# Optimization experiments

Hardware: AMD Instinct MI355X
Metric: run time of the kernel (lower is better)

The kernel has to match this reference:

```python
import jax, jax.numpy as jnp
import numpy as np

NUM_HEAD = 8

def conv1x1(x, W, b):
    # x: (n, c, h, w); W: (o, c); b: (o,)
    return jnp.einsum('nchw,oc->nohw', x, W) + b[None, :, None, None]

def setup_inputs() -> dict:
    key = jax.random.key(0)
    ks = jax.random.split(key, 9)
    n, C, H, Wd = 16, 512, 64, 64
    KC, VC = 256, 512
    s = lambda fan_in: 1.0 / np.sqrt(fan_in)
    return {
        'x':  jax.random.normal(ks[0], (n, C, H, Wd), dtype=jnp.float32),
        'Wk': jax.random.normal(ks[1], (KC, C), dtype=jnp.float32) * s(C),
        'bk': jnp.zeros((KC,), dtype=jnp.float32),
        'Wq': jax.random.normal(ks[2], (KC, C), dtype=jnp.float32) * s(C),
        'bq': jnp.zeros((KC,), dtype=jnp.float32),
        'Wv': jax.random.normal(ks[3], (VC, C), dtype=jnp.float32) * s(C),
        'bv': jnp.zeros((VC,), dtype=jnp.float32),
        'We': jax.random.normal(ks[4], (C, VC), dtype=jnp.float32) * s(VC),
        'be': jnp.zeros((C,), dtype=jnp.float32),
    }

def reference(x, Wk, bk, Wq, bq, Wv, bv, We, be):
    n, c, h, w = x.shape
    L = h * w
    Hn = NUM_HEAD
    key   = conv1x1(x, Wk, bk).reshape(n, Hn, -1, L)   # (n, H, hk, L)
    query = conv1x1(x, Wq, bq).reshape(n, Hn, -1, L)   # (n, H, hk, L)
    value = conv1x1(x, Wv, bv).reshape(n, Hn, -1, L)   # (n, H, hv, L)
    key_sm   = jax.nn.softmax(key, axis=3)              # softmax over spatial
    query_sm = jax.nn.softmax(query, axis=2)            # softmax over head channels
    # linear attention: (value @ key^T) @ query, no LxL matrix
    context = jnp.einsum('nhvl,nhkl->nhvk', value, key_sm)     # (n, H, hv, hk)
    att = jnp.einsum('nhvk,nhkl->nhvl', context, query_sm)     # (n, H, hv, L)
    att = att.reshape(n, -1, h, w)                              # (n, VC, h, w)
    return x + conv1x1(att, We, be)
```

## Files before the change

kernel.cpp:

```cpp
#include <hip/hip_runtime.h>
#include <cstddef>
#include <cstdint>

#define N_BATCH 16
#define C_IN    512
#define L       4096
#define KC      256
#define VC      512
#define NH      8
#define HK      32
#define HV      64

using f32x4 = __attribute__((ext_vector_type(4))) float;
using s16x8 = __attribute__((ext_vector_type(8))) short;

static __device__ inline ushort f2bf(float f) {
  uint32_t u = __float_as_uint(f);
  uint32_t r = (u + 0x7FFFu + ((u >> 16) & 1u)) >> 16;
  return (ushort)r;
}
static __device__ inline float bf2f(ushort u) {
  return __uint_as_float((uint32_t)u << 16);
}

__global__ __launch_bounds__(256) void k_prep_w(
    const float* __restrict__ Wk, const float* __restrict__ bk,
    const float* __restrict__ Wq, const float* __restrict__ bq,
    ushort* __restrict__ Wb, float* __restrict__ bb)
{
  const int o = blockIdx.x;
  const float* src; const float* bsrc; int oo;
  if (o < 256) { src = Wk + (size_t)o * C_IN;         bsrc = bk; oo = o; }
  else         { src = Wq + (size_t)(o - 256) * C_IN; bsrc = bq; oo = o - 256; }
  const int t = threadIdx.x;
  Wb[(size_t)o * C_IN + t * 2]     = f2bf(src[t * 2]);
  Wb[(size_t)o * C_IN + t * 2 + 1] = f2bf(src[t * 2 + 1]);
  if (t == 0) bb[o] = bsrc[oo];
}

__global__ __launch_bounds__(256) void k_prep_x(const float* __restrict__ x,
                                                ushort* __restrict__ xT,
                                                ushort* __restrict__ xb)
{
  __shared__ float t[64][65];
  const int n = blockIdx.z, cy = blockIdx.y, lx = blockIdx.x;
  const float* xp = x + ((size_t)n * C_IN + cy * 64) * L + (size_t)lx * 64;
  ushort* xbp = xb + ((size_t)n * C_IN + cy * 64) * L + (size_t)lx * 64;
  const int l4 = (threadIdx.x & 15) * 4;
  const int c0 = threadIdx.x >> 4;
  #pragma unroll
  for (int i = 0; i < 4; ++i) {
    int cc = c0 + i * 16;
    f32x4 v = *(const f32x4*)&xp[(size_t)cc * L + l4];
    t[cc][l4]     = v[0];
    t[cc][l4 + 1] = v[1];
    t[cc][l4 + 2] = v[2];
    t[cc][l4 + 3] = v[3];
    uint2 pk;
    pk.x = (uint32_t)f2bf(v[0]) | ((uint32_t)f2bf(v[1]) << 16);
    pk.y = (uint32_t)f2bf(v[2]) | ((uint32_t)f2bf(v[3]) << 16);
    *(uint2*)(xbp + (size_t)cc * L + l4) = pk;
  }
  __syncthreads();
  ushort* op = xT + ((size_t)n * L + lx * 64) * C_IN + cy * 64;
  const int cp = (threadIdx.x & 15) * 4;
  const int l0 = threadIdx.x >> 4;
  #pragma unroll
  for (int i = 0; i < 4; ++i) {
    int lr = l0 + i * 16;
    uint2 pk;
    pk.x = (uint32_t)f2bf(t[cp][lr])     | ((uint32_t)f2bf(t[cp + 1][lr]) << 16);
    pk.y = (uint32_t)f2bf(t[cp + 2][lr]) | ((uint32_t)f2bf(t[cp + 3][lr]) << 16);
    *(uint2*)(op + (size_t)lr * C_IN + cp) = pk;
  }
}

#define QBM 256
#define QBN 256
#define QBK 64

__global__ __launch_bounds__(512) void k_kq_mfma(
    const ushort* __restrict__ Wb,
    const ushort* __restrict__ xT,
    const float* __restrict__ bb,
    ushort* __restrict__ Kbuf,
    ushort* __restrict__ qT)
{
  extern __shared__ __align__(16) char smem[];
  const int n  = blockIdx.z;
  const int oy = blockIdx.y;
  const int lx = blockIdx.x;
  const int tid  = threadIdx.x;
  const int wave = tid >> 6, lane = tid & 63;
  const int wr = wave >> 2, wc = wave & 3;

  f32x4 acc[8][4] = {};

  const ushort* gA = Wb + (size_t)(oy * QBM) * C_IN;
  const ushort* gB = xT + ((size_t)n * L + lx * QBN) * C_IN;

  const int srow = lane >> 3;
  const int sslotbase = lane & 7;

  #define QSTAGE(buf, k0)                                                        \
    {                                                                            \
      ushort* As_ = (ushort*)(smem + (buf) * 65536);                             \
      ushort* Bs_ = (ushort*)(smem + (buf) * 65536 + 32768);                     \
      _Pragma("unroll")                                                          \
      for (int i_ = 0; i_ < 4; ++i_) {                                           \
        int rbase_ = wave * 32 + i_ * 8;                                         \
        int row_ = rbase_ + srow;                                                \
        int ss_ = sslotbase ^ (row_ & 7);                                        \
        __builtin_amdgcn_global_load_lds(                                        \
            (const __attribute__((address_space(1))) uint32_t*)(gA + (size_t)row_ * C_IN + (k0) + ss_ * 8), \
            (__attribute__((address_space(3))) uint32_t*)(As_ + rbase_ * QBK),   \
            16, 0, 0);                                                           \
        __builtin_amdgcn_global_load_lds(                                        \
            (const __attribute__((address_space(1))) uint32_t*)(gB + (size_t)row_ * C_IN + (k0) + ss_ * 8), \
            (__attribute__((address_space(3))) uint32_t*)(Bs_ + rbase_ * QBK),   \
            16, 0, 0);                                                           \
      }                                                                          \
    }

  QSTAGE(0, 0)
  __syncthreads();

  const int nt = C_IN / QBK;
  for (int t = 0; t < nt; ++t) {
    if (t < nt - 1) QSTAGE((t + 1) & 1, (t + 1) * QBK)
    ushort* As = (ushort*)(smem + (t & 1) * 65536);
    ushort* Bs = (ushort*)(smem + (t & 1) * 65536 + 32768);
    __builtin_amdgcn_s_setprio(1);
    #pragma unroll
    for (int ks = 0; ks < 2; ++ks) {
      s16x8 af[8], bfr[4];
      #pragma unroll
      for (int m = 0; m < 8; ++m) {
        int row = wr * 128 + m * 16 + (lane & 15);
        int slot = (ks * 4 + (lane >> 4)) ^ (row & 7);
        af[m] = *(const s16x8*)&As[row * QBK + slot * 8];
      }
      #pragma unroll
      for (int nn = 0; nn < 4; ++nn) {
        int row = wc * 64 + nn * 16 + (lane & 15);
        int slot = (ks * 4 + (lane >> 4)) ^ (row & 7);
        bfr[nn] = *(const s16x8*)&Bs[row * QBK + slot * 8];
      }
      #pragma unroll
      for (int m = 0; m < 8; ++m)
        #pragma unroll
        for (int nn = 0; nn < 4; ++nn)
          acc[m][nn] = __builtin_amdgcn_mfma_f32_16x16x32_bf16(af[m], bfr[nn], acc[m][nn], 0, 0, 0);
    }
    __builtin_amdgcn_s_setprio(0);
    __syncthreads();
  }
  #undef QSTAGE

  if (oy == 0) {
    float* ep = (float*)smem + wave * (16 * 68);
    const int erow = lane >> 4;
    const int ecol = lane & 15;
    const float* bias = bb + wr * 128;
    ushort* outp = Kbuf + ((size_t)n * 256 + wr * 128) * L
                 + (size_t)lx * QBN + wc * 64;
    #pragma unroll
    for (int m = 0; m < 8; ++m) {
      #pragma unroll
      for (int nn = 0; nn < 4; ++nn)
        #pragma unroll
        for (int r = 0; r < 4; ++r)
          ep[(erow * 4 + r) * 68 + nn * 16 + ecol] = acc[m][nn][r];
      #pragma unroll
      for (int p = 0; p < 4; ++p) {
        int row = p * 4 + erow;
        f32x4 v = *(const f32x4*)&ep[row * 68 + ecol * 4];
        float bo = bias[m * 16 + row];
        uint2 pk;
        pk.x = (uint32_t)f2bf(v[0] + bo) | ((uint32_t)f2bf(v[1] + bo) << 16);
        pk.y = (uint32_t)f2bf(v[2] + bo) | ((uint32_t)f2bf(v[3] + bo) << 16);
        *(uint2*)&outp[(size_t)(m * 16 + row) * L + ecol * 4] = pk;
      }
    }
  } else {
    const float* bias = bb + 256 + wr * 128;
    ushort* qbase = qT + (size_t)n * L * KC;
    const int g4 = (lane >> 4) * 4;
    #pragma unroll
    for (int hp = 0; hp < 4; ++hp) {
      const int m0 = 2 * hp, m1 = 2 * hp + 1;
      const float b0_0 = bias[m0 * 16 + g4 + 0], b0_1 = bias[m0 * 16 + g4 + 1];
      const float b0_2 = bias[m0 * 16 + g4 + 2], b0_3 = bias[m0 * 16 + g4 + 3];
      const float b1_0 = bias[m1 * 16 + g4 + 0], b1_1 = bias[m1 * 16 + g4 + 1];
      const float b1_2 = bias[m1 * 16 + g4 + 2], b1_3 = bias[m1 * 16 + g4 + 3];
      #pragma unroll
      for (int nn = 0; nn < 4; ++nn) {
        float v0[4], v1[4];
        v0[0] = acc[m0][nn][0] + b0_0; v0[1] = acc[m0][nn][1] + b0_1;
        v0[2] = acc[m0][nn][2] + b0_2; v0[3] = acc[m0][nn][3] + b0_3;
        v1[0] = acc[m1][nn][0] + b1_0; v1[1] = acc[m1][nn][1] + b1_1;
        v1[2] = acc[m1][nn][2] + b1_2; v1[3] = acc[m1][nn][3] + b1_3;
        float mx = fmaxf(fmaxf(fmaxf(v0[0], v0[1]), fmaxf(v0[2], v0[3])),
                         fmaxf(fmaxf(v1[0], v1[1]), fmaxf(v1[2], v1[3])));
        mx = fmaxf(mx, __shfl_xor(mx, 16));
        mx = fmaxf(mx, __shfl_xor(mx, 32));
        float e0[4], e1[4];
        float s = 0.f;
        #pragma unroll
        for (int r = 0; r < 4; ++r) { e0[r] = __expf(v0[r] - mx); s += e0[r]; }
        #pragma unroll
        for (int r = 0; r < 4; ++r) { e1[r] = __expf(v1[r] - mx); s += e1[r]; }
        s += __shfl_xor(s, 16);
        s += __shfl_xor(s, 32);
        float inv = 1.0f / s;
        int l = lx * QBN + wc * 64 + nn * 16 + (lane & 15);
        ushort* dst = qbase + (size_t)l * KC + wr * 128;
        uint2 p0, p1;
        p0.x = (uint32_t)f2bf(e0[0] * inv) | ((uint32_t)f2bf(e0[1] * inv) << 16);
        p0.y = (uint32_t)f2bf(e0[2] * inv) | ((uint32_t)f2bf(e0[3] * inv) << 16);
        p1.x = (uint32_t)f2bf(e1[0] * inv) | ((uint32_t)f2bf(e1[1] * inv) << 16);
        p1.y = (uint32_t)f2bf(e1[2] * inv) | ((uint32_t)f2bf(e1[3] * inv) << 16);
        *(uint2*)&dst[m0 * 16 + g4] = p0;
        *(uint2*)&dst[m1 * 16 + g4] = p1;
      }
    }
  }
}

__device__ inline float blockReduceMax(float v, float* red) {
  #pragma unroll
  for (int off = 32; off > 0; off >>= 1)
    v = fmaxf(v, __shfl_down(v, off, 64));
  int tid = threadIdx.x;
  if ((tid & 63) == 0) red[tid >> 6] = v;
  __syncthreads();
  return fmaxf(fmaxf(red[0], red[1]), fmaxf(red[2], red[3]));
}
__device__ inline float blockReduceSum(float v, float* red) {
  #pragma unroll
  for (int off = 32; off > 0; off >>= 1)
    v += __shfl_down(v, off, 64);
  int tid = threadIdx.x;
  if ((tid & 63) == 0) red[tid >> 6] = v;
  __syncthreads();
  return red[0] + red[1] + red[2] + red[3];
}

__global__ __launch_bounds__(256) void k_kstats3(const ushort* __restrict__ Kbuf,
                                                 float* __restrict__ kmax,
                                                 float* __restrict__ kinv)
{
  const int r = blockIdx.x;
  const int n = blockIdx.y;
  const ushort* row = Kbuf + ((size_t)n * 256 + r) * L;
  __shared__ float red1[4];
  __shared__ float red2[4];
  const int tid = threadIdx.x;
  s16x8 a = *(const s16x8*)(row + tid * 16);
  s16x8 b = *(const s16x8*)(row + tid * 16 + 8);
  float v[16];
  #pragma unroll
  for (int j = 0; j < 8; ++j) { v[j] = bf2f((ushort)a[j]); v[8 + j] = bf2f((ushort)b[j]); }
  float m = -3.0e38f;
  #pragma unroll
  for (int j = 0; j < 16; ++j) m = fmaxf(m, v[j]);
  m = blockReduceMax(m, red1);
  float s = 0.f;
  #pragma unroll
  for (int j = 0; j < 16; ++j) s += __expf(v[j] - m);
  s = blockReduceSum(s, red2);
  if (tid == 0) { kmax[n * KC + r] = m; kinv[n * KC + r] = 1.0f / s; }
}

#define GBK 64

__global__ __launch_bounds__(512) void k_G(
    const ushort* __restrict__ xb,
    const ushort* __restrict__ Kbuf,
    const float* __restrict__ kmax,
    const float* __restrict__ kinv,
    float* __restrict__ Gp)
{
  extern __shared__ __align__(16) char smem[];
  const int cm = blockIdx.x;
  const int lc = blockIdx.y;
  const int n  = blockIdx.z;
  const int tid  = threadIdx.x;
  const int wave = tid >> 6, lane = tid & 63;
  const int wr = wave >> 2, wc = wave & 3;

  f32x4 acc[4][4] = {};

  const ushort* gxb = xb   + ((size_t)n * C_IN + cm * 128) * L + lc * 1024;
  const ushort* gK  = Kbuf + (size_t)n * 256 * L + lc * 1024;

  const int brow = tid >> 1;
  const int bseg0 = (tid & 1) * 4;
  const float mk = kmax[n * KC + brow];
  const float ik = kinv[n * KC + brow];

  #define ASTAGE(buf, k0)                                                        \
    {                                                                            \
      ushort* As_ = (ushort*)(smem + (buf) * 49152);                             \
      _Pragma("unroll")                                                          \
      for (int i_ = 0; i_ < 2; ++i_) {                                           \
        int rbase_ = wave * 16 + i_ * 8;                                         \
        int row_ = rbase_ + (lane >> 3);                                         \
        int ss_ = (lane & 7) ^ (row_ & 7);                                       \
        __builtin_amdgcn_global_load_lds(                                        \
            (const __attribute__((address_space(1))) uint32_t*)(gxb + (size_t)row_ * L + (k0) + ss_ * 8), \
            (__attribute__((address_space(3))) uint32_t*)(As_ + rbase_ * GBK),   \
            16, 0, 0);                                                           \
      }                                                                          \
    }

  #define BLOAD(k0)                                                              \
    _Pragma("unroll")                                                            \
    for (int i_ = 0; i_ < 4; ++i_)                                               \
      bk[i_] = *(const s16x8*)(gK + (size_t)brow * L + (k0) + (bseg0 + i_) * 8);

  #define BWRITE(buf)                                                            \
    {                                                                            \
      ushort* Bs_ = (ushort*)(smem + (buf) * 49152 + 16384);                     \
      _Pragma("unroll")                                                          \
      for (int i_ = 0; i_ < 4; ++i_) {                                           \
        s16x8 w_;                                                                \
        _Pragma("unroll")                                                        \
        for (int j_ = 0; j_ < 8; ++j_)                                           \
          w_[j_] = (short)f2bf(__expf(bf2f((ushort)bk[i_][j_]) - mk) * ik);      \
        *(s16x8*)&Bs_[brow * GBK + ((bseg0 + i_) ^ (brow & 7)) * 8] = w_;        \
      }                                                                          \
    }

  s16x8 bk[4];

  BLOAD(0)
  ASTAGE(0, 0)
  BWRITE(0)
  __syncthreads();

  const int nt = 1024 / GBK;
  for (int t = 0; t < nt; ++t) {
    const int cb = t & 1, nb = cb ^ 1;
    if (t < nt - 1) {
      BLOAD((t + 1) * GBK)
      ASTAGE(nb, (t + 1) * GBK)
    }
    ushort* As = (ushort*)(smem + cb * 49152);
    ushort* Bs = (ushort*)(smem + cb * 49152 + 16384);
    __builtin_amdgcn_s_setprio(1);
    #pragma unroll
    for (int ks = 0; ks < 2; ++ks) {
      s16x8 af[4], bfr[4];
      #pragma unroll
      for (int m = 0; m < 4; ++m) {
        int row = wr * 64 + m * 16 + (lane & 15);
        int slot = (ks * 4 + (lane >> 4)) ^ (row & 7);
        af[m] = *(const s16x8*)&As[row * GBK + slot * 8];
      }
      #pragma unroll
      for (int nn = 0; nn < 4; ++nn) {
        int row = wc * 64 + nn * 16 + (lane & 15);
        int slot = (ks * 4 + (lane >> 4)) ^ (row & 7);
        bfr[nn] = *(const s16x8*)&Bs[row * GBK + slot * 8];
      }
      #pragma unroll
      for (int m = 0; m < 4; ++m)
        #pragma unroll
        for (int nn = 0; nn < 4; ++nn)
          acc[m][nn] = __builtin_amdgcn_mfma_f32_16x16x32_bf16(af[m], bfr[nn], acc[m][nn], 0, 0, 0);
    }
    __builtin_amdgcn_s_setprio(0);
    if (t < nt - 1) BWRITE(nb)
    __syncthreads();
  }
  #undef ASTAGE
  #undef BLOAD
  #undef BWRITE

  float* ep = (float*)smem + wave * (16 * 68);
  const int erow = lane >> 4;
  const int ecol = lane & 15;
  float* op = Gp + (((size_t)n * 4 + lc) * 512 + cm * 128 + wr * 64) * 256 + wc * 64;
  #pragma unroll
  for (int m = 0; m < 4; ++m) {
    #pragma unroll
    for (int nn = 0; nn < 4; ++nn)
      #pragma unroll
      for (int r = 0; r < 4; ++r)
        ep[(erow * 4 + r) * 68 + nn * 16 + ecol] = acc[m][nn][r];
    #pragma unroll
    for (int p = 0; p < 4; ++p) {
      int row16 = p * 4 + erow;
      f32x4 v = *(const f32x4*)&ep[row16 * 68 + ecol * 4];
      *(f32x4*)&op[(size_t)(m * 16 + row16) * 256 + ecol * 4] = v;
    }
  }
}

__global__ __launch_bounds__(256) void k_F(
    const float* __restrict__ Wv, const float* __restrict__ bv,
    const float* __restrict__ We,
    ushort* __restrict__ F, float* __restrict__ Fb)
{
  const int h  = blockIdx.x;
  const int og = blockIdx.y;
  const int tid = threadIdx.x;
  __shared__ float Ws[16][64];
  #pragma unroll
  for (int i = 0; i < 4; ++i) {
    int e = tid + i * 256;
    int o = e >> 6, v = e & 63;
    Ws[o][v] = We[(size_t)(og * 16 + o) * VC + h * 64 + v];
  }
  __syncthreads();
  const int c2 = tid * 2;
  float acc[16][2] = {};
  for (int v = 0; v < 64; ++v) {
    float2 w = *(const float2*)&Wv[(size_t)(h * 64 + v) * C_IN + c2];
    #pragma unroll
    for (int o = 0; o < 16; ++o) {
      acc[o][0] += Ws[o][v] * w.x;
      acc[o][1] += Ws[o][v] * w.y;
    }
  }
  ushort* Fh = F + ((size_t)h * 512 + og * 16) * C_IN;
  #pragma unroll
  for (int o = 0; o < 16; ++o) {
    uint32_t pk = (uint32_t)f2bf(acc[o][0]) | ((uint32_t)f2bf(acc[o][1]) << 16);
    *(uint32_t*)&Fh[(size_t)o * C_IN + c2] = pk;
  }
  if (tid < 16) {
    float s = 0.f;
    for (int v = 0; v < 64; ++v) s += Ws[tid][v] * bv[h * 64 + v];
    Fb[h * 512 + og * 16 + tid] = s;
  }
}

__global__ __launch_bounds__(256) void k_M(
    const float* __restrict__ Gp,
    const ushort* __restrict__ F,
    const float* __restrict__ Fb,
    ushort* __restrict__ Mbuf)
{
  const int oy = blockIdx.x;
  const int h  = blockIdx.y;
  const int n  = blockIdx.z;
  const int tid = threadIdx.x, wave = tid >> 6, lane = tid & 63;

  __shared__ __align__(16) char smem[32768 + 32768 + 9216];
  ushort* GTs = (ushort*)smem;

  #pragma unroll
  for (int i = 0; i < 16; ++i) {
    int e = tid + i * 256;
    int c = e >> 3, kq = e & 7;
    int k = kq * 4;
    const float* gp = Gp + ((size_t)n * 4 * 512 + c) * 256 + h * HK + k;
    f32x4 s = *(const f32x4*)gp;
    s += *(const f32x4*)(gp + (size_t)512 * 256);
    s += *(const f32x4*)(gp + (size_t)2 * 512 * 256);
    s += *(const f32x4*)(gp + (size_t)3 * 512 * 256);
    #pragma unroll
    for (int j = 0; j < 4; ++j) {
      int kk = k + j;
      GTs[kk * 512 + (((c >> 3) ^ (kk & 7)) * 8) + (c & 7)] = f2bf(s[j]);
    }
  }

  const ushort* gA = F + ((size_t)h * 512 + oy * 128) * C_IN;

  #define MSTAGE(buf, k0)                                                        \
    {                                                                            \
      ushort* As_ = (ushort*)(smem + 32768 + (buf) * 16384);                     \
      _Pragma("unroll")                                                          \
      for (int i_ = 0; i_ < 4; ++i_) {                                           \
        int rbase_ = wave * 32 + i_ * 8;                                         \
        int row_ = rbase_ + (lane >> 3);                                         \
        int ss_ = (lane & 7) ^ (row_ & 7);                                       \
        __builtin_amdgcn_global_load_lds(                                        \
            (const __attribute__((address_space(1))) uint32_t*)(gA + (size_t)row_ * C_IN + (k0) + ss_ * 8), \
            (__attribute__((address_space(3))) uint32_t*)(As_ + rbase_ * 64),    \
            16, 0, 0);                                                           \
      }                                                                          \
    }

  f32x4 acc[2][2] = {};

  MSTAGE(0, 0)
  __syncthreads();

  const int nt = C_IN / 64;
  for (int t = 0; t < nt; ++t) {
    if (t < nt - 1) MSTAGE((t + 1) & 1, (t + 1) * 64)
    ushort* As = (ushort*)(smem + 32768 + (t & 1) * 16384);
    __builtin_amdgcn_s_setprio(1);
    #pragma unroll
    for (int ks = 0; ks < 2; ++ks) {
      s16x8 af[2], bfr[2];
      #pragma unroll
      for (int m = 0; m < 2; ++m) {
        int row = wave * 32 + m * 16 + (lane & 15);
        int slot = (ks * 4 + (lane >> 4)) ^ (row & 7);
        af[m] = *(const s16x8*)&As[row * 64 + slot * 8];
      }
      #pragma unroll
      for (int nf = 0; nf < 2; ++nf) {
        int kr = nf * 16 + (lane & 15);
        int slot = (t * 8 + ks * 4 + (lane >> 4)) ^ (kr & 7);
        bfr[nf] = *(const s16x8*)&GTs[kr * 512 + slot * 8];
      }
      #pragma unroll
      for (int m = 0; m < 2; ++m)
        #pragma unroll
        for (int nf = 0; nf < 2; ++nf)
          acc[m][nf] = __builtin_amdgcn_mfma_f32_16x16x32_bf16(af[m], bfr[nf], acc[m][nf], 0, 0, 0);
    }
    __builtin_amdgcn_s_setprio(0);
    __syncthreads();
  }
  #undef MSTAGE

  float* ep = (float*)(smem + 65536) + wave * (16 * 36);
  const int erow = lane >> 4;
  const int ecol = lane & 15;
  #pragma unroll
  for (int m = 0; m < 2; ++m) {
    #pragma unroll
    for (int nf = 0; nf < 2; ++nf)
      #pragma unroll
      for (int r = 0; r < 4; ++r)
        ep[(erow * 4 + r) * 36 + nf * 16 + ecol] = acc[m][nf][r];
    #pragma unroll
    for (int p = 0; p < 2; ++p) {
      int row16 = p * 8 + (lane >> 3);
      int c4 = (lane & 7) * 4;
      f32x4 v = *(const f32x4*)&ep[row16 * 36 + c4];
      int o = oy * 128 + wave * 32 + m * 16 + row16;
      float fb = Fb[h * 512 + o];
      uint2 pk;
      pk.x = (uint32_t)f2bf(v[0] + fb) | ((uint32_t)f2bf(v[1] + fb) << 16);
      pk.y = (uint32_t)f2bf(v[2] + fb) | ((uint32_t)f2bf(v[3] + fb) << 16);
      *(uint2*)&Mbuf[((size_t)n * 512 + o) * KC + h * HK + c4] = pk;
    }
  }
}

#define BM 128
#define BN 128
#define BK 32

__global__ __launch_bounds__(256) void k_final_mfma(
    const ushort* __restrict__ Mb,
    const ushort* __restrict__ qT,
    const float* __restrict__ x,
    const float* __restrict__ be,
    float* __restrict__ out)
{
  const int n  = blockIdx.z;
  const int oy = blockIdx.y;
  const int lx = blockIdx.x;
  const int tid  = threadIdx.x;
  const int wave = tid >> 6, lane = tid & 63;
  const int wr = wave >> 1, wc = wave & 1;

  __shared__ __align__(16) char smem[32768 + 17408];

  f32x4 acc[4][4] = {};

  const ushort* gA = Mb + ((size_t)n * 512 + oy * BM) * KC;
  const ushort* gB = qT + ((size_t)n * L + lx * BN) * KC;

  const int r0 = wave * 32;
  const int lrow = lane >> 2;

  #define FSTAGE(buf, k0)                                                        \
    {                                                                            \
      ushort* As_ = (ushort*)(smem + (buf) * 16384);                             \
      ushort* Bs_ = (ushort*)(smem + (buf) * 16384 + 8192);                      \
      _Pragma("unroll")                                                          \
      for (int i_ = 0; i_ < 2; ++i_) {                                           \
        int row_ = r0 + i_ * 16 + lrow;                                          \
        int ss_ = (lane & 3) ^ ((row_ >> 1) & 3);                                \
        __builtin_amdgcn_global_load_lds(                                        \
            (const __attribute__((address_space(1))) uint32_t*)(gA + (size_t)row_ * KC + (k0) + ss_ * 8), \
            (__attribute__((address_space(3))) uint32_t*)(As_ + (r0 + i_ * 16) * BK), \
            16, 0, 0);                                                           \
        __builtin_amdgcn_global_load_lds(                                        \
            (const __attribute__((address_space(1))) uint32_t*)(gB + (size_t)row_ * KC + (k0) + ss_ * 8), \
            (__attribute__((address_space(3))) uint32_t*)(Bs_ + (r0 + i_ * 16) * BK), \
            16, 0, 0);                                                           \
      }                                                                          \
    }

  FSTAGE(0, 0)
  __syncthreads();

  const int nt = KC / BK;
  for (int t = 0; t < nt; ++t) {
    if (t < nt - 1) FSTAGE((t + 1) & 1, (t + 1) * BK)
    ushort* As = (ushort*)(smem + (t & 1) * 16384);
    ushort* Bs = (ushort*)(smem + (t & 1) * 16384 + 8192);
    s16x8 af[4], bfr[4];
    #pragma unroll
    for (int m = 0; m < 4; ++m) {
      int row = wr * 64 + m * 16 + (lane & 15);
      int slot = (lane >> 4) ^ ((row >> 1) & 3);
      af[m] = *(const s16x8*)&As[row * BK + slot * 8];
    }
    #pragma unroll
    for (int nn = 0; nn < 4; ++nn) {
      int row = wc * 64 + nn * 16 + (lane & 15);
      int slot = (lane >> 4) ^ ((row >> 1) & 3);
      bfr[nn] = *(const s16x8*)&Bs[row * BK + slot * 8];
    }
    __builtin_amdgcn_s_setprio(1);
    #pragma unroll
    for (int m = 0; m < 4; ++m)
      #pragma unroll
      for (int nn = 0; nn < 4; ++nn)
        acc[m][nn] = __builtin_amdgcn_mfma_f32_16x16x32_bf16(af[m], bfr[nn], acc[m][nn], 0, 0, 0);
    __builtin_amdgcn_s_setprio(0);
    __syncthreads();
  }
  #undef FSTAGE

  float* ep = (float*)(smem + 32768) + wave * (16 * 68);
  const int erow = lane >> 4;
  const int ecol = lane & 15;
  const float* bias = be + oy * BM + wr * 64;
  const float* xp = x + ((size_t)n * 512 + oy * BM + wr * 64) * L
                  + (size_t)lx * BN + wc * 64;
  float* op = out + ((size_t)n * 512 + oy * BM + wr * 64) * L
            + (size_t)lx * BN + wc * 64;
  #pragma unroll
  for (int m = 0; m < 4; ++m) {
    #pragma unroll
    for (int nn = 0; nn < 4; ++nn)
      #pragma unroll
      for (int r = 0; r < 4; ++r)
        ep[(erow * 4 + r) * 68 + nn * 16 + ecol] = acc[m][nn][r];
    #pragma unroll
    for (int p = 0; p < 4; ++p) {
      int row = p * 4 + erow;
      f32x4 v = *(const f32x4*)&ep[row * 68 + ecol * 4];
      float bo = bias[m * 16 + row];
      f32x4 xv = *(const f32x4*)&xp[(size_t)(m * 16 + row) * L + ecol * 4];
      v = v + xv + bo;
      *(f32x4*)&op[(size_t)(m * 16 + row) * L + ecol * 4] = v;
    }
  }
}

extern "C" void kernel_launch(void* const* d_in, const int* in_sizes, int n_in,
                              void* d_out, int out_size, void* d_ws, size_t ws_size,
                              hipStream_t stream)
{
  const float* x  = (const float*)d_in[0];
  const float* Wk = (const float*)d_in[1];
  const float* bk = (const float*)d_in[2];
  const float* Wq = (const float*)d_in[3];
  const float* bq = (const float*)d_in[4];
  const float* Wv = (const float*)d_in[5];
  const float* bv = (const float*)d_in[6];
  const float* We = (const float*)d_in[7];
  const float* be = (const float*)d_in[8];
  float* out = (float*)d_out;

  char* ws = (char*)d_ws;
  size_t off = 0;
  ushort* Kbuf = (ushort*)(ws + off); off += (size_t)N_BATCH * 256 * L * 2;
  ushort* xT   = (ushort*)(ws + off); off += (size_t)N_BATCH * L * C_IN * 2;
  ushort* xb   = (ushort*)(ws + off); off += (size_t)N_BATCH * C_IN * L * 2;
  ushort* Wb   = (ushort*)(ws + off); off += (size_t)512 * C_IN * 2;
  float*  bb   = (float*)(ws + off);  off += (size_t)512 * 4;
  float*  kmax = (float*)(ws + off);  off += (size_t)N_BATCH * KC * 4;
  float*  kinv = (float*)(ws + off);  off += (size_t)N_BATCH * KC * 4;
  ushort* qT   = (ushort*)(ws + off); off += (size_t)N_BATCH * L * KC * 2;
  float*  Gp   = (float*)(ws + off);  off += (size_t)N_BATCH * 4 * 512 * 256 * 4;
  ushort* Fbuf = (ushort*)(ws + off); off += (size_t)NH * 512 * C_IN * 2;
  float*  Fb   = (float*)(ws + off);  off += (size_t)NH * 512 * 4;
  ushort* Mbuf = (ushort*)(ws + off); off += (size_t)N_BATCH * 512 * KC * 2;

  (void)hipFuncSetAttribute((const void*)k_kq_mfma,
                            hipFuncAttributeMaxDynamicSharedMemorySize, 131072);
  (void)hipFuncSetAttribute((const void*)k_G,
                            hipFuncAttributeMaxDynamicSharedMemorySize, 98304);

  k_prep_w<<<dim3(512), 256, 0, stream>>>(Wk, bk, Wq, bq, Wb, bb);
  k_F<<<dim3(NH, 32), 256, 0, stream>>>(Wv, bv, We, Fbuf, Fb);
  k_prep_x<<<dim3(64, 8, N_BATCH), 256, 0, stream>>>(x, xT, xb);
  k_kq_mfma<<<dim3(16, 2, N_BATCH), 512, 131072, stream>>>(Wb, xT, bb, Kbuf, qT);
  k_kstats3<<<dim3(KC, N_BATCH), 256, 0, stream>>>(Kbuf, kmax, kinv);
  k_G<<<dim3(4, 4, N_BATCH), 512, 98304, stream>>>(xb, Kbuf, kmax, kinv, Gp);
  k_M<<<dim3(4, NH, N_BATCH), 256, 0, stream>>>(Gp, Fbuf, Fb, Mbuf);
  k_final_mfma<<<dim3(32, 4, N_BATCH), 256, 0, stream>>>(Mbuf, qT, x, be, out);
}
```

Before: 268.0 us.

## Drop transposed x copy; use LDS transpose reads in K/Q GEMM

Removes the transposed bf16 copy xT and makes the x preparation kernel a plain elementwise fp32-to-bf16 conversion. The K/Q GEMM now stages B tiles directly from the channel-major xb layout and builds MFMA operands with ds_read_b64_tr_b16 transpose reads from LDS. This removes one full write of the activation tensor and the shared-memory transpose pass. In exchange it adds an explicit lgkmcnt wait and a scheduling barrier inside the inner loop, and the new LDS layout could cause bank conflicts.

```diff
diff --git a/kernel.cpp b/kernel.cpp
--- a/kernel.cpp
+++ b/kernel.cpp
@@ -13,6 +13,8 @@
 
 using f32x4 = __attribute__((ext_vector_type(4))) float;
 using s16x8 = __attribute__((ext_vector_type(8))) short;
+using s16x4 = __attribute__((ext_vector_type(4))) short;
+using u32x2 = __attribute__((ext_vector_type(2))) unsigned int;
 
 static __device__ inline ushort f2bf(float f) {
   uint32_t u = __float_as_uint(f);
@@ -21,6 +23,11 @@
 }
 static __device__ inline float bf2f(ushort u) {
   return __uint_as_float((uint32_t)u << 16);
+}
+static __device__ inline s16x8 mk8(u32x2 lo, u32x2 hi) {
+  s16x4 a = __builtin_bit_cast(s16x4, lo);
+  s16x4 b = __builtin_bit_cast(s16x4, hi);
+  return __builtin_shufflevector(a, b, 0, 1, 2, 3, 4, 5, 6, 7);
 }
 
 __global__ __launch_bounds__(256) void k_prep_w(
@@ -38,50 +45,32 @@
   if (t == 0) bb[o] = bsrc[oo];
 }
 
-__global__ __launch_bounds__(256) void k_prep_x(const float* __restrict__ x,
-                                                ushort* __restrict__ xT,
-                                                ushort* __restrict__ xb)
-{
-  __shared__ float t[64][65];
-  const int n = blockIdx.z, cy = blockIdx.y, lx = blockIdx.x;
-  const float* xp = x + ((size_t)n * C_IN + cy * 64) * L + (size_t)lx * 64;
-  ushort* xbp = xb + ((size_t)n * C_IN + cy * 64) * L + (size_t)lx * 64;
-  const int l4 = (threadIdx.x & 15) * 4;
-  const int c0 = threadIdx.x >> 4;
-  #pragma unroll
-  for (int i = 0; i < 4; ++i) {
-    int cc = c0 + i * 16;
-    f32x4 v = *(const f32x4*)&xp[(size_t)cc * L + l4];
-    t[cc][l4]     = v[0];
-    t[cc][l4 + 1] = v[1];
-    t[cc][l4 + 2] = v[2];
-    t[cc][l4 + 3] = v[3];
-    uint2 pk;
-    pk.x = (uint32_t)f2bf(v[0]) | ((uint32_t)f2bf(v[1]) << 16);
-    pk.y = (uint32_t)f2bf(v[2]) | ((uint32_t)f2bf(v[3]) << 16);
-    *(uint2*)(xbp + (size_t)cc * L + l4) = pk;
-  }
-  __syncthreads();
-  ushort* op = xT + ((size_t)n * L + lx * 64) * C_IN + cy * 64;
-  const int cp = (threadIdx.x & 15) * 4;
-  const int l0 = threadIdx.x >> 4;
-  #pragma unroll
-  for (int i = 0; i < 4; ++i) {
-    int lr = l0 + i * 16;
-    uint2 pk;
-    pk.x = (uint32_t)f2bf(t[cp][lr])     | ((uint32_t)f2bf(t[cp + 1][lr]) << 16);
-    pk.y = (uint32_t)f2bf(t[cp + 2][lr]) | ((uint32_t)f2bf(t[cp + 3][lr]) << 16);
-    *(uint2*)(op + (size_t)lr * C_IN + cp) = pk;
-  }
+__global__ __launch_bounds__(256) void k_prep_xb(const float* __restrict__ x,
+                                                 ushort* __restrict__ xb)
+{
+  size_t i = ((size_t)blockIdx.x * 256 + threadIdx.x) * 8;
+  f32x4 a = *(const f32x4*)(x + i);
+  f32x4 b = *(const f32x4*)(x + i + 4);
+  s16x8 w;
+  #pragma unroll
+  for (int j = 0; j < 4; ++j) {
+    w[j]     = (short)f2bf(a[j]);
+    w[j + 4] = (short)f2bf(b[j]);
+  }
+  *(s16x8*)(xb + i) = w;
 }
 
 #define QBM 256
 #define QBN 256
 #define QBK 64
 
+#define TRRD(dst, off_lit)                                                       \
+  asm volatile("ds_read_b64_tr_b16 %0, %1 offset:" #off_lit                      \
+               : "=v"(dst) : "v"(trp));
+
 __global__ __launch_bounds__(512) void k_kq_mfma(
     const ushort* __restrict__ Wb,
-    const ushort* __restrict__ xT,
+    const ushort* __restrict__ xb,
     const float* __restrict__ bb,
     ushort* __restrict__ Kbuf,
     ushort* __restrict__ qT)
@@ -97,55 +86,75 @@
   f32x4 acc[8][4] = {};
 
   const ushort* gA = Wb + (size_t)(oy * QBM) * C_IN;
-  const ushort* gB = xT + ((size_t)n * L + lx * QBN) * C_IN;
-
-  const int srow = lane >> 3;
-  const int sslotbase = lane & 7;
-
-  #define QSTAGE(buf, k0)                                                        \
+  const ushort* gX = xb + (size_t)n * C_IN * L + (size_t)lx * QBN;
+
+  #define ASTG(buf, k0)                                                          \
     {                                                                            \
       ushort* As_ = (ushort*)(smem + (buf) * 65536);                             \
-      ushort* Bs_ = (ushort*)(smem + (buf) * 65536 + 32768);                     \
       _Pragma("unroll")                                                          \
       for (int i_ = 0; i_ < 4; ++i_) {                                           \
         int rbase_ = wave * 32 + i_ * 8;                                         \
-        int row_ = rbase_ + srow;                                                \
-        int ss_ = sslotbase ^ (row_ & 7);                                        \
+        int row_ = rbase_ + (lane >> 3);                                         \
+        int ss_ = (lane & 7) ^ (row_ & 7);                                       \
         __builtin_amdgcn_global_load_lds(                                        \
             (const __attribute__((address_space(1))) uint32_t*)(gA + (size_t)row_ * C_IN + (k0) + ss_ * 8), \
             (__attribute__((address_space(3))) uint32_t*)(As_ + rbase_ * QBK),   \
             16, 0, 0);                                                           \
+      }                                                                          \
+    }
+
+  #define BSTG(buf, k0)                                                          \
+    {                                                                            \
+      ushort* Bs_ = (ushort*)(smem + (buf) * 65536 + 32768);                     \
+      _Pragma("unroll")                                                          \
+      for (int i_ = 0; i_ < 4; ++i_) {                                           \
+        int chunk_ = i_ * 512 + tid;                                             \
+        int lh_ = chunk_ & 1, crow_ = (chunk_ >> 1) & 3;                         \
+        int c4_ = (chunk_ >> 3) & 15, l16_ = chunk_ >> 7;                        \
         __builtin_amdgcn_global_load_lds(                                        \
-            (const __attribute__((address_space(1))) uint32_t*)(gB + (size_t)row_ * C_IN + (k0) + ss_ * 8), \
-            (__attribute__((address_space(3))) uint32_t*)(Bs_ + rbase_ * QBK),   \
+            (const __attribute__((address_space(1))) uint32_t*)(gX + (size_t)((k0) + c4_ * 4 + crow_) * L + l16_ * 16 + lh_ * 8), \
+            (__attribute__((address_space(3))) uint32_t*)(Bs_ + (i_ * 512 + wave * 64) * 8), \
             16, 0, 0);                                                           \
       }                                                                          \
     }
 
-  QSTAGE(0, 0)
+  ASTG(0, 0)
+  BSTG(0, 0)
   __syncthreads();
 
   const int nt = C_IN / QBK;
   for (int t = 0; t < nt; ++t) {
-    if (t < nt - 1) QSTAGE((t + 1) & 1, (t + 1) * QBK)
+    if (t < nt - 1) {
+      ASTG((t + 1) & 1, (t + 1) * QBK)
+      BSTG((t + 1) & 1, (t + 1) * QBK)
+    }
     ushort* As = (ushort*)(smem + (t & 1) * 65536);
     ushort* Bs = (ushort*)(smem + (t & 1) * 65536 + 32768);
     __builtin_amdgcn_s_setprio(1);
     #pragma unroll
     for (int ks = 0; ks < 2; ++ks) {
-      s16x8 af[8], bfr[4];
+      s16x8 af[8];
       #pragma unroll
       for (int m = 0; m < 8; ++m) {
         int row = wr * 128 + m * 16 + (lane & 15);
         int slot = (ks * 4 + (lane >> 4)) ^ (row & 7);
         af[m] = *(const s16x8*)&As[row * QBK + slot * 8];
       }
-      #pragma unroll
-      for (int nn = 0; nn < 4; ++nn) {
-        int row = wc * 64 + nn * 16 + (lane & 15);
-        int slot = (ks * 4 + (lane >> 4)) ^ (row & 7);
-        bfr[nn] = *(const s16x8*)&Bs[row * QBK + slot * 8];
-      }
+      const int trb = wc * 8192 + ks * 1024 + (lane >> 4) * 256 + (lane & 15) * 2;
+      __attribute__((address_space(3))) char* trp =
+          (__attribute__((address_space(3))) char*)Bs + trb;
+      u32x2 lo0, hi0, lo1, hi1, lo2, hi2, lo3, hi3;
+      TRRD(lo0, 0)    TRRD(hi0, 128)
+      TRRD(lo1, 2048) TRRD(hi1, 2176)
+      TRRD(lo2, 4096) TRRD(hi2, 4224)
+      TRRD(lo3, 6144) TRRD(hi3, 6272)
+      asm volatile("s_waitcnt lgkmcnt(0)" ::: "memory");
+      __builtin_amdgcn_sched_barrier(0);
+      s16x8 bfr[4];
+      bfr[0] = mk8(lo0, hi0);
+      bfr[1] = mk8(lo1, hi1);
+      bfr[2] = mk8(lo2, hi2);
+      bfr[3] = mk8(lo3, hi3);
       #pragma unroll
       for (int m = 0; m < 8; ++m)
         #pragma unroll
@@ -155,7 +164,8 @@
     __builtin_amdgcn_s_setprio(0);
     __syncthreads();
   }
-  #undef QSTAGE
+  #undef ASTG
+  #undef BSTG
 
   if (oy == 0) {
     float* ep = (float*)smem + wave * (16 * 68);
@@ -670,7 +680,6 @@
   char* ws = (char*)d_ws;
   size_t off = 0;
   ushort* Kbuf = (ushort*)(ws + off); off += (size_t)N_BATCH * 256 * L * 2;
-  ushort* xT   = (ushort*)(ws + off); off += (size_t)N_BATCH * L * C_IN * 2;
   ushort* xb   = (ushort*)(ws + off); off += (size_t)N_BATCH * C_IN * L * 2;
   ushort* Wb   = (ushort*)(ws + off); off += (size_t)512 * C_IN * 2;
   float*  bb   = (float*)(ws + off);  off += (size_t)512 * 4;
@@ -689,8 +698,8 @@
 
   k_prep_w<<<dim3(512), 256, 0, stream>>>(Wk, bk, Wq, bq, Wb, bb);
   k_F<<<dim3(NH, 32), 256, 0, stream>>>(Wv, bv, We, Fbuf, Fb);
-  k_prep_x<<<dim3(64, 8, N_BATCH), 256, 0, stream>>>(x, xT, xb);
-  k_kq_mfma<<<dim3(16, 2, N_BATCH), 512, 131072, stream>>>(Wb, xT, bb, Kbuf, qT);
+  k_prep_xb<<<dim3(16384), 256, 0, stream>>>(x, xb);
+  k_kq_mfma<<<dim3(16, 2, N_BATCH), 512, 131072, stream>>>(Wb, xb, bb, Kbuf, qT);
   k_kstats3<<<dim3(KC, N_BATCH), 256, 0, stream>>>(Kbuf, kmax, kinv);
   k_G<<<dim3(4, 4, N_BATCH), 512, 98304, stream>>>(xb, Kbuf, kmax, kinv, Gp);
   k_M<<<dim3(4, NH, N_BATCH), 256, 0, stream>>>(Gp, Fbuf, Fb, Mbuf);
```

After: 242.0 us. 9.7% less time.
